# Kernel optimization log

Measured on AMD Instinct MI355X. Metric: run time of the kernel, lower is better.

## Reference

```python
import jax, jax.numpy as jnp
import numpy as np

B = 32
H = W = 64
C = 128
HEADS = 4
HEAD_DIM = C // HEADS
WS = 8            # window_size
SS = 4            # shift_size
N = WS * WS       # tokens per window
MLP_HID = 4 * C
SCALE = HEAD_DIM ** -0.5
EPS = 1e-5


def _rel_pos_index():
    coords = np.stack(np.meshgrid(np.arange(WS), np.arange(WS), indexing='ij'))
    cf = coords.reshape(2, -1)
    rel = (cf[:, :, None] - cf[:, None, :]).transpose(1, 2, 0)
    rel[:, :, 0] += WS - 1
    rel[:, :, 1] += WS - 1
    rel[:, :, 0] *= 2 * WS - 1
    return rel.sum(-1)  # (N, N) int


def _attn_mask():
    img_mask = np.zeros((1, H, W, 1), np.float32)
    slices = (slice(0, -WS), slice(-WS, -SS), slice(-SS, None))
    cnt = 0
    for hs in slices:
        for ws in slices:
            img_mask[:, hs, ws, :] = cnt
            cnt += 1
    mw = img_mask.reshape(1, H // WS, WS, W // WS, WS, 1)
    mw = mw.transpose(0, 1, 3, 2, 4, 5).reshape(-1, N)  # (nW, N)
    am = mw[:, None, :] - mw[:, :, None]
    return np.where(am != 0, np.float32(-100.0), np.float32(0.0))  # (nW, N, N)


REL_POS_IDX = jnp.asarray(_rel_pos_index().reshape(-1))  # (N*N,)
ATTN_MASK = jnp.asarray(_attn_mask())                    # (nW, N, N)


def setup_inputs() -> dict:
    key = jax.random.key(0)
    ks = jax.random.split(key, 12)
    s = 0.02
    return {
        'x': jax.random.normal(ks[0], (B, H * W, C), jnp.float32),
        'norm1_g': jnp.ones((C,), jnp.float32),
        'norm1_b': jnp.zeros((C,), jnp.float32),
        'qkv_w': jax.random.normal(ks[1], (C, 3 * C), jnp.float32) * s,
        'qkv_b': jnp.zeros((3 * C,), jnp.float32),
        'proj_w': jax.random.normal(ks[2], (C, C), jnp.float32) * s,
        'proj_b': jnp.zeros((C,), jnp.float32),
        'rpb_table': jax.random.normal(ks[3], ((2 * WS - 1) * (2 * WS - 1), HEADS), jnp.float32) * s,
        'norm2_g': jnp.ones((C,), jnp.float32),
        'norm2_b': jnp.zeros((C,), jnp.float32),
        'mlp_w1': jax.random.normal(ks[4], (C, MLP_HID), jnp.float32) * s,
        'mlp_b1': jnp.zeros((MLP_HID,), jnp.float32),
        'mlp_w2': jax.random.normal(ks[5], (MLP_HID, C), jnp.float32) * s,
        'mlp_b2': jnp.zeros((C,), jnp.float32),
    }


def _layernorm(x, g, b):
    m = x.mean(-1, keepdims=True)
    v = jnp.mean((x - m) ** 2, -1, keepdims=True)
    return (x - m) * jax.lax.rsqrt(v + EPS) * g + b


def reference(x, norm1_g, norm1_b, qkv_w, qkv_b, proj_w, proj_b, rpb_table,
              norm2_g, norm2_b, mlp_w1, mlp_b1, mlp_w2, mlp_b2):
    shortcut = x
    h = _layernorm(x, norm1_g, norm1_b).reshape(-1, H, W, C)
    # cyclic shift
    h = jnp.roll(h, (-SS, -SS), axis=(1, 2))
    # window partition -> (B*nW, N, C)
    hw = h.reshape(-1, H // WS, WS, W // WS, WS, C)
    hw = hw.transpose(0, 1, 3, 2, 4, 5).reshape(-1, N, C)
    # window attention
    qkv = (hw @ qkv_w + qkv_b).reshape(-1, N, 3, HEADS, HEAD_DIM)
    qkv = qkv.transpose(2, 0, 3, 1, 4)  # (3, B*nW, heads, N, hd)
    q, k, v = qkv[0] * SCALE, qkv[1], qkv[2]
    attn = jnp.einsum('bhnd,bhmd->bhnm', q, k)  # (B*nW, heads, N, N)
    rpb = rpb_table[REL_POS_IDX].reshape(N, N, HEADS).transpose(2, 0, 1)
    attn = attn + rpb[None]
    nW = ATTN_MASK.shape[0]
    attn = attn.reshape(-1, nW, HEADS, N, N) + ATTN_MASK[None, :, None]
    attn = jax.nn.softmax(attn.reshape(-1, HEADS, N, N), axis=-1)
    out = jnp.einsum('bhnm,bhmd->bhnd', attn, v)
    out = out.transpose(0, 2, 1, 3).reshape(-1, N, C)
    out = out @ proj_w + proj_b
    # window reverse
    out = out.reshape(-1, H // WS, W // WS, WS, WS, C)
    out = out.transpose(0, 1, 3, 2, 4, 5).reshape(-1, H, W, C)
    # reverse cyclic shift
    out = jnp.roll(out, (SS, SS), axis=(1, 2)).reshape(-1, H * W, C)
    x = shortcut + out
    # MLP branch
    h2 = _layernorm(x, norm2_g, norm2_b)
    h2 = jax.nn.gelu(h2 @ mlp_w1 + mlp_b1, approximate=False)
    h2 = h2 @ mlp_w2 + mlp_b2
    return x + h2
```

## Files before the change

### kernel.cpp

```cpp
#include <hip/hip_runtime.h>
#include <math.h>

typedef __attribute__((ext_vector_type(8))) short bf16x8;
typedef __attribute__((ext_vector_type(4))) short bf16x4;
typedef __attribute__((ext_vector_type(4))) float f32x4;
typedef __attribute__((ext_vector_type(4))) unsigned short u16x4;

#define DEVI __device__ __forceinline__

DEVI float b2f(unsigned int u){ union{unsigned int i; float f;} c; c.i = u<<16; return c.f; }
DEVI unsigned short f2b(float f){
  union{float f; unsigned int i;} c; c.f = f;
  unsigned int r = c.i + 0x7fffu + ((c.i>>16)&1u);
  return (unsigned short)(r>>16);
}
DEVI unsigned int pack2(float a, float b){
  return (unsigned int)f2b(a) | ((unsigned int)f2b(b)<<16);
}
DEVI void unpack8(uint4 u, float* f){
  f[0]=b2f(u.x&0xffffu); f[1]=b2f(u.x>>16);
  f[2]=b2f(u.y&0xffffu); f[3]=b2f(u.y>>16);
  f[4]=b2f(u.z&0xffffu); f[5]=b2f(u.z>>16);
  f[6]=b2f(u.w&0xffffu); f[7]=b2f(u.w>>16);
}
DEVI f32x4 mfma16(bf16x8 a, bf16x8 b, f32x4 c){
  return __builtin_amdgcn_mfma_f32_16x16x32_bf16(a, b, c, 0, 0, 0);
}
DEVI f32x4 mfma16x16(bf16x4 a, bf16x4 b, f32x4 c){
#if __has_builtin(__builtin_amdgcn_mfma_f32_16x16x16bf16_1k)
  return __builtin_amdgcn_mfma_f32_16x16x16bf16_1k(a, b, c, 0, 0, 0);
#else
  f32x4 d = c;
  asm volatile("v_mfma_f32_16x16x16_bf16 %0, %1, %2, %0" : "+v"(d) : "v"(a), "v"(b));
  return d;
#endif
}
DEVI float gelu_fast(float u){
  const float y2 = 1.5957691216057308f*(u + 0.044715f*u*u*u);
  return u / (1.f + __expf(-y2));
}
DEVI int swzA(int row, int byi){ return row*256 + (byi ^ ((row&7)<<4)); }
DEVI int swzQ(int row, int byi){ return row*64  + (byi ^ (((row>>1)&3)<<4)); }
DEVI int swzO(int row, int byc){ return row*512 + (byc ^ ((row&7)<<4) ^ (((byc>>7)&3)<<5)); }

__global__ void k_prep(const float* __restrict__ qkvw, const float* __restrict__ projw,
                       const float* __restrict__ w1,   const float* __restrict__ w2,
                       const float* __restrict__ rpbt,
                       ushort* __restrict__ qkvF, ushort* __restrict__ projF,
                       ushort* __restrict__ w1F,  ushort* __restrict__ w2F,
                       ushort* __restrict__ rpbE)
{
  const int t = blockIdx.x*256 + threadIdx.x;
  const int l = t&63, fr = t>>6;
  const int l15 = l&15, l4 = l>>4;
  {
    const int head = t>>12, q = (t>>6)&63, k = t&63;
    const int di = (q>>3)-(k>>3)+7, dj = (q&7)-(k&7)+7;
    rpbE[t] = f2b(rpbt[(di*15+dj)*4 + head]);
  }
  {
    const int c = fr>>5, og = (fr>>2)&7, h = fr&3;
    const int oc = og*16 + l15, hid0 = c*64 + h*16 + l4*4;
    ushort* d = w2F + (size_t)fr*256 + l*4;
    #pragma unroll
    for(int e=0;e<4;e++) d[e] = f2b(w2[(size_t)(hid0+e)*128 + oc]);
  }
  if (fr < 128){
    const int c = fr>>4, hg = (fr>>2)&3, kk = fr&3;
    const int hid = c*64 + hg*16 + l15, k0 = kk*32 + l4*8;
    ushort* d = w1F + (size_t)fr*512 + l*8;
    #pragma unroll
    for(int e=0;e<8;e++) d[e] = f2b(w1[(size_t)(k0+e)*512 + hid]);
  }
  if (fr < 96){
    const int s3 = fr>>5, g = (fr>>2)&7, kk = fr&3;
    const int col = s3*128 + g*16 + l15, k0 = kk*32 + l4*8;
    ushort* d = qkvF + (size_t)fr*512 + l*8;
    #pragma unroll
    for(int e=0;e<8;e++) d[e] = f2b(qkvw[(size_t)(k0+e)*384 + col]);
  }
  if (fr < 32){
    const int g = fr>>2, kk = fr&3;
    const int col = g*16 + l15, k0 = kk*32 + l4*8;
    ushort* d = projF + (size_t)fr*512 + l*8;
    #pragma unroll
    for(int e=0;e<8;e++) d[e] = f2b(projw[(size_t)(k0+e)*128 + col]);
  }
}

__global__ __launch_bounds__(256,3) void k_attn(
    const float*  __restrict__ x,
    const float*  __restrict__ g1, const float* __restrict__ be1,
    const ushort* __restrict__ qkvF, const float* __restrict__ qkvb,
    const ushort* __restrict__ projF, const float* __restrict__ projb,
    const ushort* __restrict__ rpbE,
    ushort* __restrict__ x2w)
{
  __shared__ __align__(16) char smem[49152];
  const int tid  = threadIdx.x;
  const int wave = tid>>6, lane = tid&63;
  const int l15 = lane&15, l4 = lane>>4;
  const int wid = blockIdx.x;
  const int b   = wid>>6, wim = wid&63;
  const int wh  = wim>>3, wv = wim&7;

  char* const smA  = smem;
  char* const smQ  = smem + 16384 + wave*8192;
  char* const smK  = smQ + 4096;
  char* const smR  = smem + 16384;

  const f32x4 Z = {0.f,0.f,0.f,0.f};
  const int t_row = tid>>2;
  const int cg    = (tid&3)*32;
  const int ti_r = t_row>>3, tj_r = t_row&7;
  const int ho_r = (wh*8+ti_r+4)&63, wo_r = (wv*8+tj_r+4)&63;
  const size_t growbase = ((size_t)(b*4096 + ho_r*64 + wo_r))*128;

  float xraw[32];

  {
    const float* src = x + growbase + cg;
    #pragma unroll
    for(int q=0;q<8;q++){
      const float4 f4 = *(const float4*)(src + q*4);
      xraw[q*4+0]=f4.x; xraw[q*4+1]=f4.y; xraw[q*4+2]=f4.z; xraw[q*4+3]=f4.w;
    }
    float s=0.f, ss=0.f;
    #pragma unroll
    for(int e=0;e<32;e++){ s+=xraw[e]; ss+=xraw[e]*xraw[e]; }
    s += __shfl_xor(s,1); ss += __shfl_xor(ss,1);
    s += __shfl_xor(s,2); ss += __shfl_xor(ss,2);
    const float mean = s*(1.f/128.f);
    const float varv = fmaxf(ss*(1.f/128.f) - mean*mean, 0.f);
    const float rstd = rsqrtf(varv + 1e-5f);
    #pragma unroll
    for(int q=0;q<4;q++){
      const float4 ga = *(const float4*)(g1 +cg+q*8);
      const float4 gb = *(const float4*)(g1 +cg+q*8+4);
      const float4 ba = *(const float4*)(be1+cg+q*8);
      const float4 bb = *(const float4*)(be1+cg+q*8+4);
      const float* vp = xraw + q*8;
      uint4 pk;
      pk.x = pack2((vp[0]-mean)*rstd*ga.x+ba.x, (vp[1]-mean)*rstd*ga.y+ba.y);
      pk.y = pack2((vp[2]-mean)*rstd*ga.z+ba.z, (vp[3]-mean)*rstd*ga.w+ba.w);
      pk.z = pack2((vp[4]-mean)*rstd*gb.x+bb.x, (vp[5]-mean)*rstd*gb.y+bb.y);
      pk.w = pack2((vp[6]-mean)*rstd*gb.z+bb.z, (vp[7]-mean)*rstd*gb.w+bb.w);
      *(uint4*)(smA + swzA(t_row, cg*2 + q*16)) = pk;
    }
  }
  __syncthreads();

  const int headc = wave*32;
  bf16x4 Vf[4][2];

  {
    #pragma unroll
    for(int s3=0;s3<3;s3++){
      f32x4 acc[4][2];
      #pragma unroll
      for(int rt=0;rt<4;rt++){ acc[rt][0]=Z; acc[rt][1]=Z; }
      bf16x8 bfr[2][4];
      #pragma unroll
      for(int ct=0;ct<2;ct++)
        #pragma unroll
        for(int kk=0;kk<4;kk++)
          bfr[ct][kk] = *(const bf16x8*)(qkvF + (size_t)((s3*8 + wave*2 + ct)*4 + kk)*512 + lane*8);
      #pragma unroll
      for(int kk=0;kk<4;kk++){
        bf16x8 afr[4];
        #pragma unroll
        for(int rt=0;rt<4;rt++)
          afr[rt] = *(const bf16x8*)(smA + swzA(rt*16+l15, kk*64 + l4*16));
        #pragma unroll
        for(int rt=0;rt<4;rt++)
          #pragma unroll
          for(int ct=0;ct<2;ct++)
            acc[rt][ct] = mfma16(afr[rt], bfr[ct][kk], acc[rt][ct]);
      }
      #pragma unroll
      for(int ct=0;ct<2;ct++){
        const int hd = ct*16 + l15;
        const float bias = qkvb[s3*128 + headc + hd];
        if (s3==2){
          #pragma unroll
          for(int rt=0;rt<4;rt++){
            union { uint2 u; bf16x4 v; } cv;
            cv.u.x = pack2(acc[rt][ct][0]+bias, acc[rt][ct][1]+bias);
            cv.u.y = pack2(acc[rt][ct][2]+bias, acc[rt][ct][3]+bias);
            Vf[rt][ct] = cv.v;
          }
        } else {
          char* const dst = (s3==0) ? smQ : smK;
          const float sc = (s3==0) ? 0.17677669529663687f : 1.f;
          #pragma unroll
          for(int rt=0;rt<4;rt++){
            const int t0 = rt*16 + l4*4;
            #pragma unroll
            for(int j=0;j<4;j++)
              *(ushort*)(dst + swzQ(t0+j, hd*2)) = f2b((acc[rt][ct][j]+bias)*sc);
          }
        }
      }
    }
  }
  __syncthreads();

  f32x4 O[4][2];
  #pragma unroll
  for(int rt=0;rt<4;rt++){ O[rt][0]=Z; O[rt][1]=Z; }
  {
    bf16x8 kfr[4];
    #pragma unroll
    for(int g=0; g<4; ++g)
      kfr[g] = *(const bf16x8*)(smK + swzQ(g*16+l15, l4*16));
    const bool edge = (wh==7) || (wv==7);
    #pragma unroll
    for(int rt=0; rt<4; ++rt){
      const bf16x8 qf = *(const bf16x8*)(smQ + swzQ(rt*16+l15, l4*16));
      f32x4 S[4];
      #pragma unroll
      for(int g=0; g<4; ++g)
        S[g] = mfma16(kfr[g], qf, Z);
      const int q = rt*16 + l15;
      int regq = 0;
      if (edge){
        const int qi=q>>3, qj=q&7;
        regq = ((wh<7)?0:((qi<4)?1:2))*3 + ((wv<7)?0:((qj<4)?1:2));
      }
      const ushort* rbase = rpbE + wave*4096 + q*64 + l4*4;
      #pragma unroll
      for(int g=0; g<4; ++g){
        const u16x4 rb = *(const u16x4*)(rbase + g*16);
        #pragma unroll
        for(int j=0;j<4;j++){
          float add = b2f(rb[j]);
          if (edge){
            const int k = g*16 + l4*4 + j;
            const int ki=k>>3, kj=k&7;
            const int regk = ((wh<7)?0:((ki<4)?1:2))*3 + ((wv<7)?0:((kj<4)?1:2));
            if (regk != regq) add -= 100.f;
          }
          S[g][j] += add;
        }
      }
      float mx = -1e30f;
      #pragma unroll
      for(int g=0;g<4;g++)
        #pragma unroll
        for(int j=0;j<4;j++) mx = fmaxf(mx, S[g][j]);
      mx = fmaxf(mx, __shfl_xor(mx,16));
      mx = fmaxf(mx, __shfl_xor(mx,32));
      float sm = 0.f;
      #pragma unroll
      for(int g=0;g<4;g++)
        #pragma unroll
        for(int j=0;j<4;j++){ const float e = __expf(S[g][j]-mx); S[g][j]=e; sm+=e; }
      sm += __shfl_xor(sm,16);
      sm += __shfl_xor(sm,32);
      const float inv = 1.f/sm;
      #pragma unroll
      for(int g=0;g<4;g++){
        union { uint2 u; bf16x4 v; } cv;
        cv.u.x = pack2(S[g][0]*inv, S[g][1]*inv);
        cv.u.y = pack2(S[g][2]*inv, S[g][3]*inv);
        #pragma unroll
        for(int cvi=0;cvi<2;cvi++)
          O[rt][cvi] = mfma16x16(cv.v, Vf[g][cvi], O[rt][cvi]);
      }
    }
    #pragma unroll
    for(int rt=0;rt<4;rt++)
      #pragma unroll
      for(int cvi=0;cvi<2;cvi++)
        #pragma unroll
        for(int j=0;j<4;j++)
          *(ushort*)(smA + swzA(rt*16+l4*4+j, (headc + cvi*16 + l15)*2)) = f2b(O[rt][cvi][j]);
  }
  __syncthreads();

  {
    f32x4 PR[4][2];
    #pragma unroll
    for(int rt=0;rt<4;rt++){ PR[rt][0]=Z; PR[rt][1]=Z; }
    bf16x8 pb[2][4];
    #pragma unroll
    for(int ct=0;ct<2;ct++)
      #pragma unroll
      for(int kk=0;kk<4;kk++)
        pb[ct][kk] = *(const bf16x8*)(projF + (size_t)((wave*2+ct)*4 + kk)*512 + lane*8);
    #pragma unroll
    for(int kk=0;kk<4;kk++){
      bf16x8 afr[4];
      #pragma unroll
      for(int rt=0;rt<4;rt++)
        afr[rt] = *(const bf16x8*)(smA + swzA(rt*16+l15, kk*64 + l4*16));
      #pragma unroll
      for(int rt=0;rt<4;rt++)
        #pragma unroll
        for(int ct=0;ct<2;ct++)
          PR[rt][ct] = mfma16(afr[rt], pb[ct][kk], PR[rt][ct]);
    }
    #pragma unroll
    for(int ct=0;ct<2;ct++){
      const int col = headc + ct*16 + l15;
      const float bias = projb[col];
      #pragma unroll
      for(int rt=0;rt<4;rt++)
        #pragma unroll
        for(int j=0;j<4;j++)
          *(float*)(smR + swzO(rt*16+l4*4+j, col*4)) = PR[rt][ct][j] + bias;
    }
  }
  __syncthreads();

  {
    ushort* drow = x2w + ((size_t)(wid*64 + t_row))*128 + cg;
    #pragma unroll
    for(int q=0;q<4;q++){
      const f32x4 oa = *(const f32x4*)(smR + swzO(t_row, (cg+q*8  )*4));
      const f32x4 ob = *(const f32x4*)(smR + swzO(t_row, (cg+q*8+4)*4));
      const float* vp = xraw + q*8;
      uint4 pk;
      pk.x = pack2(oa[0]+vp[0], oa[1]+vp[1]);
      pk.y = pack2(oa[2]+vp[2], oa[3]+vp[3]);
      pk.z = pack2(ob[0]+vp[4], ob[1]+vp[5]);
      pk.w = pack2(ob[2]+vp[6], ob[3]+vp[7]);
      *(uint4*)(drow + q*8) = pk;
    }
  }
}

__global__ __launch_bounds__(1024) void k_mlp2(
    const ushort* __restrict__ x2w,
    const float* __restrict__ g2, const float* __restrict__ be2,
    const ushort* __restrict__ w1F, const float* __restrict__ bb1,
    const ushort* __restrict__ w2F, const float* __restrict__ bb2,
    float* __restrict__ outp)
{
  extern __shared__ __align__(16) char smem[];
  float* const smB1 = (float*)(smem + 98304);
  const int tid  = threadIdx.x;
  const int wave = tid>>6, lane = tid&63;
  const int l15 = lane&15, l4 = lane>>4;
  const int gblk = blockIdx.x;
  const f32x4 Z = {0.f,0.f,0.f,0.f};

  if (tid < 512) smB1[tid] = bb1[tid];

  {
    const int tk = tid>>2;
    const int cg = (tid&3)*32;
    const ushort* src = x2w + ((size_t)(gblk*256 + tk))*128 + cg;
    float v[32];
    unpack8(*(const uint4*)(src   ), v   );
    unpack8(*(const uint4*)(src+ 8), v+ 8);
    unpack8(*(const uint4*)(src+16), v+16);
    unpack8(*(const uint4*)(src+24), v+24);
    float s=0.f, ss=0.f;
    #pragma unroll
    for(int e=0;e<32;e++){ s+=v[e]; ss+=v[e]*v[e]; }
    s += __shfl_xor(s,1); ss += __shfl_xor(ss,1);
    s += __shfl_xor(s,2); ss += __shfl_xor(ss,2);
    const float mean = s*(1.f/128.f);
    const float varv = fmaxf(ss*(1.f/128.f) - mean*mean, 0.f);
    const float rstd = rsqrtf(varv + 1e-5f);
    #pragma unroll
    for(int q=0;q<4;q++){
      const float4 ga = *(const float4*)(g2 +cg+q*8);
      const float4 gb = *(const float4*)(g2 +cg+q*8+4);
      const float4 ba = *(const float4*)(be2+cg+q*8);
      const float4 bb = *(const float4*)(be2+cg+q*8+4);
      const float* vp = v + q*8;
      uint4 pk;
      pk.x = pack2((vp[0]-mean)*rstd*ga.x+ba.x, (vp[1]-mean)*rstd*ga.y+ba.y);
      pk.y = pack2((vp[2]-mean)*rstd*ga.z+ba.z, (vp[3]-mean)*rstd*ga.w+ba.w);
      pk.z = pack2((vp[4]-mean)*rstd*gb.x+bb.x, (vp[5]-mean)*rstd*gb.y+bb.y);
      pk.w = pack2((vp[6]-mean)*rstd*gb.z+bb.z, (vp[7]-mean)*rstd*gb.w+bb.w);
      *(uint4*)(smem + swzA(tk, cg*2 + q*16)) = pk;
    }
  }
  __syncthreads();

  const int trow = wave*16 + l15;
  bf16x8 xf[4];
  #pragma unroll
  for(int kk=0;kk<4;++kk)
    xf[kk] = *(const bf16x8*)(smem + swzA(trow, kk*64 + l4*16));
  __syncthreads();

  const ushort* const wsrc = (wave<8) ? w1F : w2F;
  const int ldsoff = ((wave<8)?0:16384) + (wave&7)*2048;
  const int subsh  = (wave&7)*1024;
  #define STAGE_CHUNK(cc, bufbase) do{ \
    const ushort* gsrc = wsrc + (size_t)(cc)*8192 + subsh + lane*8; \
    char* lb = (bufbase) + ldsoff; \
    __builtin_amdgcn_global_load_lds((const unsigned int*)(gsrc     ), (unsigned int*)(lb      ), 16, 0, 0); \
    __builtin_amdgcn_global_load_lds((const unsigned int*)(gsrc+512 ), (unsigned int*)(lb+1024 ), 16, 0, 0); \
  }while(0)

  STAGE_CHUNK(0, smem);
  STAGE_CHUNK(1, smem + 32768);

  f32x4 OA[8];
  #pragma unroll
  for(int ocg=0;ocg<8;++ocg) OA[ocg]=Z;

  for (int c=0; c<8; ++c){
    if (c < 7) asm volatile("s_waitcnt vmcnt(2)" ::: "memory");
    else       asm volatile("s_waitcnt vmcnt(0)" ::: "memory");
    __builtin_amdgcn_s_barrier();
    __builtin_amdgcn_sched_barrier(0);
    if (c < 6) STAGE_CHUNK(c+2, smem + 32768*((c+2)%3));

    char* const buf = smem + 32768*(c%3);
    const int hidb = c*64;
    f32x4 acc1[4] = {Z,Z,Z,Z};
    #pragma unroll
    for(int hg=0; hg<4; ++hg)
      #pragma unroll
      for(int kk=0; kk<4; ++kk){
        const bf16x8 wf = *(const bf16x8*)(buf + (hg*4+kk)*1024 + lane*16);
        acc1[hg] = mfma16(wf, xf[kk], acc1[hg]);
      }
    bf16x4 Hf[4];
    #pragma unroll
    for(int hg=0; hg<4; ++hg){
      const float4 b4 = *(const float4*)(&smB1[hidb + hg*16 + l4*4]);
      bf16x4 hv;
      hv[0] = (short)f2b(gelu_fast(acc1[hg][0]+b4.x));
      hv[1] = (short)f2b(gelu_fast(acc1[hg][1]+b4.y));
      hv[2] = (short)f2b(gelu_fast(acc1[hg][2]+b4.z));
      hv[3] = (short)f2b(gelu_fast(acc1[hg][3]+b4.w));
      Hf[hg] = hv;
    }
    #pragma unroll
    for(int ocg=0; ocg<8; ++ocg)
      #pragma unroll
      for(int hg=0; hg<4; ++hg){
        const bf16x4 w2f = *(const bf16x4*)(buf + 16384 + (ocg*4+hg)*512 + lane*8);
        OA[ocg] = mfma16x16(w2f, Hf[hg], OA[ocg]);
      }
    __builtin_amdgcn_sched_barrier(0);
  }
  #undef STAGE_CHUNK

  __syncthreads();
  {
    const int tk = tid>>2;
    const int cg = (tid&3)*32;
    const uint4* src = (const uint4*)(x2w + ((size_t)(gblk*256 + tk))*128 + cg);
    #pragma unroll
    for(int q=0;q<4;q++) *(uint4*)(smem + swzA(tk, cg*2 + q*16)) = src[q];
  }
  __syncthreads();
  {
    const int tk  = trow;
    const int wid = gblk*4 + (tk>>6);
    const int n   = tk & 63;
    const int bb  = wid>>6, wim = wid&63;
    const int wh  = wim>>3, wv = wim&7;
    const int ti  = n>>3,  tj = n&7;
    const int ho  = (wh*8+ti+4)&63, wo = (wv*8+tj+4)&63;
    float* const drow = outp + ((size_t)(bb*4096 + ho*64 + wo))*128;
    #pragma unroll
    for(int ocg=0; ocg<8; ++ocg){
      const int oc = ocg*16 + l4*4;
      const float4 b4 = *(const float4*)(bb2 + oc);
      const u16x4 xr = *(const u16x4*)(smem + swzA(tk, oc*2));
      f32x4 r = OA[ocg];
      r[0] += b4.x + b2f(xr[0]);
      r[1] += b4.y + b2f(xr[1]);
      r[2] += b4.z + b2f(xr[2]);
      r[3] += b4.w + b2f(xr[3]);
      *(f32x4*)(drow + oc) = r;
    }
  }
}

extern "C" void kernel_launch(void* const* d_in, const int* in_sizes, int n_in,
                              void* d_out, int out_size, void* d_ws, size_t ws_size,
                              hipStream_t stream) {
  (void)in_sizes; (void)n_in; (void)out_size; (void)ws_size;
  const float* x     = (const float*)d_in[0];
  const float* n1g   = (const float*)d_in[1];
  const float* n1b   = (const float*)d_in[2];
  const float* qkvw  = (const float*)d_in[3];
  const float* qkvb  = (const float*)d_in[4];
  const float* projw = (const float*)d_in[5];
  const float* projb = (const float*)d_in[6];
  const float* rpbt  = (const float*)d_in[7];
  const float* n2g   = (const float*)d_in[8];
  const float* n2b   = (const float*)d_in[9];
  const float* w1    = (const float*)d_in[10];
  const float* b1    = (const float*)d_in[11];
  const float* w2    = (const float*)d_in[12];
  const float* b2    = (const float*)d_in[13];
  float* outp = (float*)d_out;

  ushort* ws    = (ushort*)d_ws;
  ushort* x2w   = ws;
  ushort* qkvF  = ws + 16777216;
  ushort* projF = qkvF + 49152;
  ushort* w1F   = projF + 16384;
  ushort* w2F   = w1F + 65536;
  ushort* rpbE  = w2F + 65536;

  k_prep<<<64, 256, 0, stream>>>(qkvw, projw, w1, w2, rpbt, qkvF, projF, w1F, w2F, rpbE);
  k_attn<<<2048, 256, 0, stream>>>(x, n1g, n1b, qkvF, qkvb, projF, projb, rpbE, x2w);
  k_mlp2<<<512, 1024, 100352, stream>>>(x2w, n2g, n2b, w1F, b1, w2F, b2, outp);
}
```

Baseline: 173.3 us.

## Keep Q and K in registers via transposed MFMA instead of LDS round-trip

Computes Q and K projections with swapped MFMA operands so the accumulator layout directly matches the operand layout needed for the QK^T product. Q and K are then held in registers as bf16x4 fragments, and the scores use two 16x16x16 MFMAs per tile instead of one 16x16x32. This removes the scalar ushort stores of Q/K to LDS and the reads that followed. In exchange it uses more registers and issues twice as many, smaller MFMAs for the scores, which could reduce occupancy.

```diff
diff --git a/kernel.cpp b/kernel.cpp
--- a/kernel.cpp
+++ b/kernel.cpp
@@ -40,7 +40,6 @@
   return u / (1.f + __expf(-y2));
 }
 DEVI int swzA(int row, int byi){ return row*256 + (byi ^ ((row&7)<<4)); }
-DEVI int swzQ(int row, int byi){ return row*64  + (byi ^ (((row>>1)&3)<<4)); }
 DEVI int swzO(int row, int byc){ return row*512 + (byc ^ ((row&7)<<4) ^ (((byc>>7)&3)<<5)); }
 
 __global__ void k_prep(const float* __restrict__ qkvw, const float* __restrict__ projw,
@@ -105,8 +104,6 @@
   const int wh  = wim>>3, wv = wim&7;
 
   char* const smA  = smem;
-  char* const smQ  = smem + 16384 + wave*8192;
-  char* const smK  = smQ + 4096;
   char* const smR  = smem + 16384;
 
   const f32x4 Z = {0.f,0.f,0.f,0.f};
@@ -151,11 +148,46 @@
   __syncthreads();
 
   const int headc = wave*32;
-  bf16x4 Vf[4][2];
-
-  {
-    #pragma unroll
-    for(int s3=0;s3<3;s3++){
+  bf16x4 Qr[4][2], Kr[4][2], Vf[4][2];
+
+  {
+    #pragma unroll
+    for(int s3=0;s3<2;s3++){
+      f32x4 acc[4][2];
+      #pragma unroll
+      for(int tg=0;tg<4;tg++){ acc[tg][0]=Z; acc[tg][1]=Z; }
+      bf16x8 wfr[2][4];
+      #pragma unroll
+      for(int ct=0;ct<2;ct++)
+        #pragma unroll
+        for(int kk=0;kk<4;kk++)
+          wfr[ct][kk] = *(const bf16x8*)(qkvF + (size_t)((s3*8 + wave*2 + ct)*4 + kk)*512 + lane*8);
+      #pragma unroll
+      for(int kk=0;kk<4;kk++){
+        bf16x8 xfr[4];
+        #pragma unroll
+        for(int tg=0;tg<4;tg++)
+          xfr[tg] = *(const bf16x8*)(smA + swzA(tg*16+l15, kk*64 + l4*16));
+        #pragma unroll
+        for(int tg=0;tg<4;tg++)
+          #pragma unroll
+          for(int ct=0;ct<2;ct++)
+            acc[tg][ct] = mfma16(wfr[ct][kk], xfr[tg], acc[tg][ct]);
+      }
+      const float sc = (s3==0) ? 0.17677669529663687f : 1.f;
+      #pragma unroll
+      for(int ct=0;ct<2;ct++){
+        const float4 b4 = *(const float4*)(qkvb + s3*128 + headc + ct*16 + l4*4);
+        #pragma unroll
+        for(int tg=0;tg<4;tg++){
+          union { uint2 u; bf16x4 v; } cv;
+          cv.u.x = pack2((acc[tg][ct][0]+b4.x)*sc, (acc[tg][ct][1]+b4.y)*sc);
+          cv.u.y = pack2((acc[tg][ct][2]+b4.z)*sc, (acc[tg][ct][3]+b4.w)*sc);
+          if (s3==0) Qr[tg][ct] = cv.v; else Kr[tg][ct] = cv.v;
+        }
+      }
+    }
+    {
       f32x4 acc[4][2];
       #pragma unroll
       for(int rt=0;rt<4;rt++){ acc[rt][0]=Z; acc[rt][1]=Z; }
@@ -164,7 +196,7 @@
       for(int ct=0;ct<2;ct++)
         #pragma unroll
         for(int kk=0;kk<4;kk++)
-          bfr[ct][kk] = *(const bf16x8*)(qkvF + (size_t)((s3*8 + wave*2 + ct)*4 + kk)*512 + lane*8);
+          bfr[ct][kk] = *(const bf16x8*)(qkvF + (size_t)((16 + wave*2 + ct)*4 + kk)*512 + lane*8);
       #pragma unroll
       for(int kk=0;kk<4;kk++){
         bf16x8 afr[4];
@@ -179,26 +211,13 @@
       }
       #pragma unroll
       for(int ct=0;ct<2;ct++){
-        const int hd = ct*16 + l15;
-        const float bias = qkvb[s3*128 + headc + hd];
-        if (s3==2){
-          #pragma unroll
-          for(int rt=0;rt<4;rt++){
-            union { uint2 u; bf16x4 v; } cv;
-            cv.u.x = pack2(acc[rt][ct][0]+bias, acc[rt][ct][1]+bias);
-            cv.u.y = pack2(acc[rt][ct][2]+bias, acc[rt][ct][3]+bias);
-            Vf[rt][ct] = cv.v;
-          }
-        } else {
-          char* const dst = (s3==0) ? smQ : smK;
-          const float sc = (s3==0) ? 0.17677669529663687f : 1.f;
-          #pragma unroll
-          for(int rt=0;rt<4;rt++){
-            const int t0 = rt*16 + l4*4;
-            #pragma unroll
-            for(int j=0;j<4;j++)
-              *(ushort*)(dst + swzQ(t0+j, hd*2)) = f2b((acc[rt][ct][j]+bias)*sc);
-          }
+        const float bias = qkvb[256 + headc + ct*16 + l15];
+        #pragma unroll
+        for(int rt=0;rt<4;rt++){
+          union { uint2 u; bf16x4 v; } cv;
+          cv.u.x = pack2(acc[rt][ct][0]+bias, acc[rt][ct][1]+bias);
+          cv.u.y = pack2(acc[rt][ct][2]+bias, acc[rt][ct][3]+bias);
+          Vf[rt][ct] = cv.v;
         }
       }
     }
@@ -209,18 +228,16 @@
   #pragma unroll
   for(int rt=0;rt<4;rt++){ O[rt][0]=Z; O[rt][1]=Z; }
   {
-    bf16x8 kfr[4];
-    #pragma unroll
-    for(int g=0; g<4; ++g)
-      kfr[g] = *(const bf16x8*)(smK + swzQ(g*16+l15, l4*16));
     const bool edge = (wh==7) || (wv==7);
     #pragma unroll
     for(int rt=0; rt<4; ++rt){
-      const bf16x8 qf = *(const bf16x8*)(smQ + swzQ(rt*16+l15, l4*16));
       f32x4 S[4];
       #pragma unroll
       for(int g=0; g<4; ++g)
-        S[g] = mfma16(kfr[g], qf, Z);
+        S[g] = mfma16x16(Kr[g][0], Qr[rt][0], Z);
+      #pragma unroll
+      for(int g=0; g<4; ++g)
+        S[g] = mfma16x16(Kr[g][1], Qr[rt][1], S[g]);
       const int q = rt*16 + l15;
       int regq = 0;
       if (edge){
```

Result: slower. 188.4 us (+8.7%).
